# Performance work log

Measured on AMD Instinct MI355X. Metric: run time of the kernel, lower is better.

## Reference

```python
import jax, jax.numpy as jnp
import numpy as np

N_NODES = 100000
E_RAW = 3200000
IN_CH = 256
HID = 128
OUT = 64
N_LAYERS = 4


def setup_inputs() -> dict:
    rng = np.random.default_rng(0)
    src = rng.integers(0, N_NODES, E_RAW)
    dst = rng.integers(0, N_NODES, E_RAW)
    # drop self loops (add_self_loops appends them explicitly) and dedupe so the
    # edge list is coalesced (torch sparse .pow acts on coalesced values)
    code = src.astype(np.int64) * N_NODES + dst.astype(np.int64)
    code = np.unique(code[src != dst])
    edge_index = jnp.asarray(np.stack([code // N_NODES, code % N_NODES]), dtype=jnp.int32)

    key = jax.random.key(0)
    ks = jax.random.split(key, 6)
    stdv = 1.0 / np.sqrt(HID)
    x = jax.random.normal(ks[0], (N_NODES, IN_CH), jnp.float32)
    W_lin1 = jax.random.uniform(ks[1], (IN_CH, HID), jnp.float32, -stdv, stdv)
    b_lin1 = jnp.zeros((HID,), jnp.float32)
    W1 = jax.random.uniform(ks[2], (N_LAYERS, HID, HID), jnp.float32, -stdv, stdv)
    W2 = jax.random.uniform(ks[3], (N_LAYERS, HID, HID), jnp.float32, -stdv, stdv)
    W_lin2 = jax.random.uniform(ks[4], (HID, OUT), jnp.float32, -stdv, stdv)
    b_lin2 = jnp.zeros((OUT,), jnp.float32)
    return {"x": x, "W_lin1": W_lin1, "b_lin1": b_lin1, "W1": W1, "W2": W2,
            "W_lin2": W_lin2, "b_lin2": b_lin2, "edge_index": edge_index}


def reference(x, W_lin1, b_lin1, W1, W2, W_lin2, b_lin2, edge_index):
    n = N_NODES
    diag = jnp.arange(n, dtype=edge_index.dtype)
    # add self loops (appended last, so diagonal entries are the final n slots)
    row = jnp.concatenate([edge_index[0], diag])
    col = jnp.concatenate([edge_index[1], diag])
    deg = jax.ops.segment_sum(jnp.ones_like(row, jnp.float32), row, num_segments=n)
    inv_deg_row = 1.0 / deg[row]                     # per-edge 1/deg(src)
    a_vals = inv_deg_row                             # A_rw = D^{-1} A (incl. self loops)
    l_vals = (-inv_deg_row).at[-n:].add(1.0)         # L_rw = I - D^{-1} A (coalesced)

    def spmm(vals, X):
        return jax.ops.segment_sum(vals[:, None] * X[col], row, num_segments=n)

    h = jax.nn.relu(x @ W_lin1 + b_lin1)
    acc = jnp.zeros((n, HID), h.dtype)
    for l in range(N_LAYERS):
        o1 = h @ W1[l]
        o2 = h @ W2[l]
        if l != 0:
            # torch sparse .pow(l) = elementwise power of nonzero values
            o1 = spmm(l_vals ** l, o1)
            o2 = spmm(a_vals ** l, o2)
        if l != N_LAYERS - 1:
            o1 = spmm(a_vals, o1)
            o2 = spmm(l_vals, o2)
        acc = acc + jax.nn.relu(o1) + jax.nn.relu(o2)
    xm = acc / (2 * N_LAYERS)
    return xm @ W_lin2 + b_lin2
```

## Files before the change

### kernel.cpp

```cpp
#include <hip/hip_runtime.h>
#include <hip/hip_bf16.h>
#include <stdint.h>

#define NN   100000
#define ICH  256
#define HID  128
#define OUTF 64

typedef float  f32x4  __attribute__((ext_vector_type(4)));
typedef __bf16 bf16x8 __attribute__((ext_vector_type(8)));

__device__ __forceinline__ float bf2f(uint16_t u){
  union { uint32_t i; float f; } v; v.i = ((uint32_t)u) << 16; return v.f;
}
__device__ __forceinline__ uint16_t f2bf(float f){
  union { float f; uint32_t i; } v; v.f = f;
  uint32_t i = v.i;
  return (uint16_t)((i + 0x7FFFu + ((i >> 16) & 1u)) >> 16);
}
__device__ __forceinline__ uint32_t pack2(float a, float b){
  return (uint32_t)f2bf(a) | ((uint32_t)f2bf(b) << 16);
}

__global__ void k_csr(const int* __restrict__ row, int E, int n,
                      int* __restrict__ rp, float* __restrict__ r){
  int i = blockIdx.x * blockDim.x + threadIdx.x;
  if (i > n) return;
  int lo = 0, hi = E;
  while (lo < hi){
    int mid = (lo + hi) >> 1;
    if (row[mid] < i) lo = mid + 1; else hi = mid;
  }
  rp[i] = lo;
  if (i < n){
    int lo2 = lo, hi2 = E;
    while (lo2 < hi2){
      int mid = (lo2 + hi2) >> 1;
      if (row[mid] < i + 1) lo2 = mid + 1; else hi2 = mid;
    }
    r[i] = 1.0f / (float)(lo2 - lo + 1);
  }
}

__global__ void k_wprep(const float* __restrict__ W1, const float* __restrict__ W2,
                        const float* __restrict__ Wl1, const float* __restrict__ Wl2,
                        uint16_t* __restrict__ W1T, uint16_t* __restrict__ W2T,
                        uint16_t* __restrict__ Wl1T, uint16_t* __restrict__ Wl2T){
  int idx = blockIdx.x * blockDim.x + threadIdx.x;
  if (idx < 4 * 128 * 128){
    int l = idx >> 14, rem = idx & 16383, n = rem >> 7, k = rem & 127;
    W1T[idx] = f2bf(W1[l * 16384 + k * 128 + n]);
    W2T[idx] = f2bf(W2[l * 16384 + k * 128 + n]);
  }
  if (idx < 128 * 256){
    int n = idx >> 8, k = idx & 255;
    Wl1T[idx] = f2bf(Wl1[k * 128 + n]);
  }
  if (idx < 64 * 128){
    int n = idx >> 7, k = idx & 127;
    Wl2T[idx] = f2bf(Wl2[k * 64 + n]);
  }
}

__launch_bounds__(256)
__global__ void k_lin1m(const float* __restrict__ x, const uint16_t* __restrict__ Wl1T,
                        const float* __restrict__ b, uint16_t* __restrict__ h){
  __shared__ __align__(16) uint16_t Xs[64][264];
  const int tid = threadIdx.x;
  const int node0 = blockIdx.x * 64;
  const int wv = tid >> 6, lane = tid & 63, lr = lane & 15, lg = lane >> 4;

  #pragma unroll
  for (int i = 0; i < 16; ++i){
    int fi = tid + i * 256;
    int rrow = fi >> 6, c4 = (fi & 63) * 4;
    int nd = node0 + rrow;
    float4 f = (nd < NN) ? *(const float4*)(x + (size_t)nd * ICH + c4)
                         : make_float4(0.f, 0.f, 0.f, 0.f);
    *(uint2*)&Xs[rrow][c4] = make_uint2(pack2(f.x, f.y), pack2(f.z, f.w));
  }
  __syncthreads();

  bf16x8 bfr[2][8];
  #pragma unroll
  for (int n2 = 0; n2 < 2; ++n2){
    const int n = (2 * wv + n2) * 16 + lr;
    const uint16_t* bp = Wl1T + (size_t)n * 256 + lg * 8;
    #pragma unroll
    for (int ks = 0; ks < 8; ++ks)
      bfr[n2][ks] = __builtin_bit_cast(bf16x8, *(const uint4*)(bp + ks * 32));
  }
  float bias[2] = {b[(2 * wv + 0) * 16 + lr], b[(2 * wv + 1) * 16 + lr]};

  #pragma unroll
  for (int rt = 0; rt < 4; ++rt){
    const int row = rt * 16 + lr;
    bf16x8 af[8];
    #pragma unroll
    for (int ks = 0; ks < 8; ++ks)
      af[ks] = __builtin_bit_cast(bf16x8, *(const uint4*)&Xs[row][ks * 32 + lg * 8]);
    #pragma unroll
    for (int n2 = 0; n2 < 2; ++n2){
      f32x4 d = (f32x4){0.f, 0.f, 0.f, 0.f};
      #pragma unroll
      for (int ks = 0; ks < 8; ++ks)
        d = __builtin_amdgcn_mfma_f32_16x16x32_bf16(af[ks], bfr[n2][ks], d, 0, 0, 0);
      const int ncol = (2 * wv + n2) * 16 + lr;
      #pragma unroll
      for (int q = 0; q < 4; ++q){
        int nd = node0 + rt * 16 + lg * 4 + q;
        if (nd < NN){
          float v = d[q] + bias[n2];
          h[(size_t)nd * HID + ncol] = f2bf(v > 0.f ? v : 0.f);
        }
      }
    }
  }
}

__launch_bounds__(256)
__global__ void k_spmmA(const int* __restrict__ col, const int* __restrict__ rp,
                        const float* __restrict__ r, const uint32_t* __restrict__ h,
                        uint32_t* __restrict__ P, uint32_t* __restrict__ T1,
                        uint32_t* __restrict__ T2){
  int wid  = (blockIdx.x * blockDim.x + threadIdx.x) >> 6;
  int lane = threadIdx.x & 63;
  if (wid >= NN) return;
  int e0 = rp[wid], e1 = rp[wid + 1];
  float a0 = 0, b0 = 0, a1 = 0, b1 = 0, a2 = 0, b2 = 0;
  for (int base = e0; base < e1; base += 64){
    int tot = e1 - base;
    int cnt = tot < 64 ? tot : 64;
    int jv  = (lane < cnt) ? col[base + lane] : 0;
    int rvb = (lane < cnt) ? __builtin_bit_cast(int, r[jv]) : 0;
    int k = 0;
    if (cnt >= 16){
      uint32_t A[16], B[16];
      #pragma unroll
      for (int t = 0; t < 16; ++t){
        int j = __builtin_amdgcn_readlane(jv, t);
        A[t] = h[((uint32_t)j << 6) + lane];
      }
      while (k + 32 <= cnt){
        #pragma unroll
        for (int t = 0; t < 16; ++t){
          int j = __builtin_amdgcn_readlane(jv, k + 16 + t);
          B[t] = h[((uint32_t)j << 6) + lane];
        }
        #pragma unroll
        for (int t = 0; t < 16; ++t){
          float rj = __builtin_bit_cast(float, __builtin_amdgcn_readlane(rvb, k + t));
          float r2 = rj * rj;
          float x0 = __builtin_bit_cast(float, A[t] << 16);
          float x1 = __builtin_bit_cast(float, A[t] & 0xFFFF0000u);
          a0 += x0;               b0 += x1;
          a1 = fmaf(rj, x0, a1);  b1 = fmaf(rj, x1, b1);
          a2 = fmaf(r2, x0, a2);  b2 = fmaf(r2, x1, b2);
        }
        #pragma unroll
        for (int t = 0; t < 16; ++t) A[t] = B[t];
        k += 16;
      }
      #pragma unroll
      for (int t = 0; t < 16; ++t){
        float rj = __builtin_bit_cast(float, __builtin_amdgcn_readlane(rvb, k + t));
        float r2 = rj * rj;
        float x0 = __builtin_bit_cast(float, A[t] << 16);
        float x1 = __builtin_bit_cast(float, A[t] & 0xFFFF0000u);
        a0 += x0;               b0 += x1;
        a1 = fmaf(rj, x0, a1);  b1 = fmaf(rj, x1, b1);
        a2 = fmaf(r2, x0, a2);  b2 = fmaf(r2, x1, b2);
      }
      k += 16;
    }
    for (; k + 4 <= cnt; k += 4){
      uint32_t hv[4];
      #pragma unroll
      for (int t = 0; t < 4; ++t){
        int j = __builtin_amdgcn_readlane(jv, k + t);
        hv[t] = h[((uint32_t)j << 6) + lane];
      }
      #pragma unroll
      for (int t = 0; t < 4; ++t){
        float rj = __builtin_bit_cast(float, __builtin_amdgcn_readlane(rvb, k + t));
        float r2 = rj * rj;
        float x0 = __builtin_bit_cast(float, hv[t] << 16);
        float x1 = __builtin_bit_cast(float, hv[t] & 0xFFFF0000u);
        a0 += x0;               b0 += x1;
        a1 = fmaf(rj, x0, a1);  b1 = fmaf(rj, x1, b1);
        a2 = fmaf(r2, x0, a2);  b2 = fmaf(r2, x1, b2);
      }
    }
    for (; k < cnt; ++k){
      int j = __builtin_amdgcn_readlane(jv, k);
      float rj = __builtin_bit_cast(float, __builtin_amdgcn_readlane(rvb, k));
      float r2 = rj * rj;
      uint32_t hv = h[((uint32_t)j << 6) + lane];
      float x0 = __builtin_bit_cast(float, hv << 16);
      float x1 = __builtin_bit_cast(float, hv & 0xFFFF0000u);
      a0 += x0;               b0 += x1;
      a1 = fmaf(rj, x0, a1);  b1 = fmaf(rj, x1, b1);
      a2 = fmaf(r2, x0, a2);  b2 = fmaf(r2, x1, b2);
    }
  }
  size_t o = (size_t)wid * 64 + lane;
  P[o]  = pack2(a0, b0);
  T1[o] = pack2(a1, b1);
  T2[o] = pack2(a2, b2);
}

__launch_bounds__(256)
__global__ void k_spmmB(const int* __restrict__ col, const int* __restrict__ rp,
                        const float* __restrict__ r, const uint32_t* __restrict__ Pm,
                        uint32_t* __restrict__ Q1, uint32_t* __restrict__ Q2){
  int wid  = (blockIdx.x * blockDim.x + threadIdx.x) >> 6;
  int lane = threadIdx.x & 63;
  if (wid >= NN) return;
  int e0 = rp[wid], e1 = rp[wid + 1];
  float a1 = 0, b1 = 0, a2 = 0, b2 = 0;
  for (int base = e0; base < e1; base += 64){
    int tot = e1 - base;
    int cnt = tot < 64 ? tot : 64;
    int jv  = (lane < cnt) ? col[base + lane] : 0;
    int rvb = (lane < cnt) ? __builtin_bit_cast(int, r[jv]) : 0;
    int k = 0;
    if (cnt >= 16){
      uint32_t A[16], B[16];
      #pragma unroll
      for (int t = 0; t < 16; ++t){
        int j = __builtin_amdgcn_readlane(jv, t);
        A[t] = Pm[((uint32_t)j << 6) + lane];
      }
      while (k + 32 <= cnt){
        #pragma unroll
        for (int t = 0; t < 16; ++t){
          int j = __builtin_amdgcn_readlane(jv, k + 16 + t);
          B[t] = Pm[((uint32_t)j << 6) + lane];
        }
        #pragma unroll
        for (int t = 0; t < 16; ++t){
          float rj = __builtin_bit_cast(float, __builtin_amdgcn_readlane(rvb, k + t));
          float r2 = rj * rj;
          float x0 = __builtin_bit_cast(float, A[t] << 16);
          float x1 = __builtin_bit_cast(float, A[t] & 0xFFFF0000u);
          a1 = fmaf(rj, x0, a1);  b1 = fmaf(rj, x1, b1);
          a2 = fmaf(r2, x0, a2);  b2 = fmaf(r2, x1, b2);
        }
        #pragma unroll
        for (int t = 0; t < 16; ++t) A[t] = B[t];
        k += 16;
      }
      #pragma unroll
      for (int t = 0; t < 16; ++t){
        float rj = __builtin_bit_cast(float, __builtin_amdgcn_readlane(rvb, k + t));
        float r2 = rj * rj;
        float x0 = __builtin_bit_cast(float, A[t] << 16);
        float x1 = __builtin_bit_cast(float, A[t] & 0xFFFF0000u);
        a1 = fmaf(rj, x0, a1);  b1 = fmaf(rj, x1, b1);
        a2 = fmaf(r2, x0, a2);  b2 = fmaf(r2, x1, b2);
      }
      k += 16;
    }
    for (; k + 4 <= cnt; k += 4){
      uint32_t pv[4];
      #pragma unroll
      for (int t = 0; t < 4; ++t){
        int j = __builtin_amdgcn_readlane(jv, k + t);
        pv[t] = Pm[((uint32_t)j << 6) + lane];
      }
      #pragma unroll
      for (int t = 0; t < 4; ++t){
        float rj = __builtin_bit_cast(float, __builtin_amdgcn_readlane(rvb, k + t));
        float r2 = rj * rj;
        float x0 = __builtin_bit_cast(float, pv[t] << 16);
        float x1 = __builtin_bit_cast(float, pv[t] & 0xFFFF0000u);
        a1 = fmaf(rj, x0, a1);  b1 = fmaf(rj, x1, b1);
        a2 = fmaf(r2, x0, a2);  b2 = fmaf(r2, x1, b2);
      }
    }
    for (; k < cnt; ++k){
      int j = __builtin_amdgcn_readlane(jv, k);
      float rj = __builtin_bit_cast(float, __builtin_amdgcn_readlane(rvb, k));
      float r2 = rj * rj;
      uint32_t pv = Pm[((uint32_t)j << 6) + lane];
      float x0 = __builtin_bit_cast(float, pv << 16);
      float x1 = __builtin_bit_cast(float, pv & 0xFFFF0000u);
      a1 = fmaf(rj, x0, a1);  b1 = fmaf(rj, x1, b1);
      a2 = fmaf(r2, x0, a2);  b2 = fmaf(r2, x1, b2);
    }
  }
  size_t o = (size_t)wid * 64 + lane;
  Q1[o] = pack2(a1, b1);
  Q2[o] = pack2(a2, b2);
}

__launch_bounds__(512)
__global__ void k_epi8(const uint32_t* __restrict__ h,  const uint32_t* __restrict__ P,
                       const uint32_t* __restrict__ T1, const uint32_t* __restrict__ T2,
                       const uint32_t* __restrict__ Q1, const uint32_t* __restrict__ Q2,
                       const float* __restrict__ r,
                       const uint16_t* __restrict__ W1T, const uint16_t* __restrict__ W2T,
                       const uint16_t* __restrict__ Wl2T, const float* __restrict__ b2,
                       float* __restrict__ out){
  __shared__ __align__(16) uint32_t Mu[2][2][64][68];
  const int tid = threadIdx.x;
  const int node0 = blockIdx.x * 64;
  const int wv = tid >> 6, lane = tid & 63, lr = lane & 15, lg = lane >> 4;

  const int nb = tid >> 3;
  const int qc = tid & 7;
  const int nd = node0 + nb;
  const int rn = nd < NN ? nd : NN - 1;
  const float rv = r[rn];
  const size_t ub = (size_t)rn * 64;
  const int cc2[2] = {qc, qc + 8};

  f32x4 acc[4];
  #pragma unroll
  for (int rt = 0; rt < 4; ++rt) acc[rt] = (f32x4){0.f, 0.f, 0.f, 0.f};

  auto mfma_phase = [&](int buf, const uint16_t* Wa, const uint16_t* Wb){
    __builtin_amdgcn_s_setprio(1);
    #pragma unroll
    for (int m = 0; m < 2; ++m){
      const uint16_t* bp = (m ? Wb : Wa) + (size_t)(wv * 16 + lr) * 128 + lg * 8;
      bf16x8 bfr[4];
      #pragma unroll
      for (int ks = 0; ks < 4; ++ks)
        bfr[ks] = __builtin_bit_cast(bf16x8, *(const uint4*)(bp + ks * 32));
      #pragma unroll
      for (int rt = 0; rt < 4; ++rt){
        const int row = rt * 16 + lr;
        f32x4 d = (f32x4){0.f, 0.f, 0.f, 0.f};
        #pragma unroll
        for (int ks = 0; ks < 4; ++ks){
          bf16x8 af = __builtin_bit_cast(bf16x8,
              *(const uint4*)&Mu[buf][m][row][ks * 16 + lg * 4]);
          d = __builtin_amdgcn_mfma_f32_16x16x32_bf16(af, bfr[ks], d, 0, 0, 0);
        }
        #pragma unroll
        for (int q = 0; q < 4; ++q)
          acc[rt][q] += (d[q] > 0.f ? d[q] : 0.f);
      }
    }
    __builtin_amdgcn_s_setprio(0);
  };

  uint4 vh[2], vP[2], vT1[2], vQ1[2];
  #pragma unroll
  for (int ci = 0; ci < 2; ++ci){
    vh[ci]  = *(const uint4*)(h  + ub + cc2[ci] * 4);
    vP[ci]  = *(const uint4*)(P  + ub + cc2[ci] * 4);
    vT1[ci] = *(const uint4*)(T1 + ub + cc2[ci] * 4);
    vQ1[ci] = *(const uint4*)(Q1 + ub + cc2[ci] * 4);
  }

  #pragma unroll
  for (int ci = 0; ci < 2; ++ci){
    const uint32_t* ah = (const uint32_t*)&vh[ci];
    const uint32_t* ap = (const uint32_t*)&vP[ci];
    uint32_t o1[4], o2[4];
    #pragma unroll
    for (int w = 0; w < 4; ++w){
      float m1s[2], m2s[2];
      #pragma unroll
      for (int s = 0; s < 2; ++s){
        float hh = bf2f((uint16_t)(s ? (ah[w] >> 16) : ah[w]));
        float pp = bf2f((uint16_t)(s ? (ap[w] >> 16) : ap[w]));
        float F = rv * (pp + hh);
        m1s[s] = F; m2s[s] = hh - F;
      }
      o1[w] = pack2(m1s[0], m1s[1]);
      o2[w] = pack2(m2s[0], m2s[1]);
    }
    *(uint4*)&Mu[0][0][nb][cc2[ci] * 4] = make_uint4(o1[0], o1[1], o1[2], o1[3]);
    *(uint4*)&Mu[0][1][nb][cc2[ci] * 4] = make_uint4(o2[0], o2[1], o2[2], o2[3]);
  }
  __syncthreads();

  mfma_phase(0, W1T, W2T);
  #pragma unroll
  for (int ci = 0; ci < 2; ++ci){
    const uint32_t* ah = (const uint32_t*)&vh[ci];
    const uint32_t* ap = (const uint32_t*)&vP[ci];
    const uint32_t* at = (const uint32_t*)&vT1[ci];
    const uint32_t* aq = (const uint32_t*)&vQ1[ci];
    uint32_t o1[4], o2[4];
    #pragma unroll
    for (int w = 0; w < 4; ++w){
      float m1s[2], m2s[2];
      #pragma unroll
      for (int s = 0; s < 2; ++s){
        float hh = bf2f((uint16_t)(s ? (ah[w] >> 16) : ah[w]));
        float pp = bf2f((uint16_t)(s ? (ap[w] >> 16) : ap[w]));
        float t1 = bf2f((uint16_t)(s ? (at[w] >> 16) : at[w]));
        float q1 = bf2f((uint16_t)(s ? (aq[w] >> 16) : aq[w]));
        float F = rv * (pp + hh);
        float G = hh - F;
        m1s[s] = rv * (pp - q1 - t1 + G);
        m2s[s] = F - rv * (q1 + t1 + F);
      }
      o1[w] = pack2(m1s[0], m1s[1]);
      o2[w] = pack2(m2s[0], m2s[1]);
    }
    *(uint4*)&Mu[1][0][nb][cc2[ci] * 4] = make_uint4(o1[0], o1[1], o1[2], o1[3]);
    *(uint4*)&Mu[1][1][nb][cc2[ci] * 4] = make_uint4(o2[0], o2[1], o2[2], o2[3]);
  }
  uint4 vT2[2], vQ2[2];
  #pragma unroll
  for (int ci = 0; ci < 2; ++ci){
    vT2[ci] = *(const uint4*)(T2 + ub + cc2[ci] * 4);
    vQ2[ci] = *(const uint4*)(Q2 + ub + cc2[ci] * 4);
  }
  __syncthreads();

  mfma_phase(1, W1T + 16384, W2T + 16384);
  #pragma unroll
  for (int ci = 0; ci < 2; ++ci){
    const uint32_t* ah = (const uint32_t*)&vh[ci];
    const uint32_t* ap = (const uint32_t*)&vP[ci];
    const uint32_t* at1 = (const uint32_t*)&vT1[ci];
    const uint32_t* at2 = (const uint32_t*)&vT2[ci];
    const uint32_t* aq2 = (const uint32_t*)&vQ2[ci];
    uint32_t o1[4], o2[4];
    #pragma unroll
    for (int w = 0; w < 4; ++w){
      float m1s[2], m2s[2];
      #pragma unroll
      for (int s = 0; s < 2; ++s){
        float hh = bf2f((uint16_t)(s ? (ah[w] >> 16) : ah[w]));
        float pp = bf2f((uint16_t)(s ? (ap[w] >> 16) : ap[w]));
        float t1 = bf2f((uint16_t)(s ? (at1[w] >> 16) : at1[w]));
        float t2 = bf2f((uint16_t)(s ? (at2[w] >> 16) : at2[w]));
        float q2 = bf2f((uint16_t)(s ? (aq2[w] >> 16) : aq2[w]));
        float omr = 1.f - rv;
        float G2 = rv * rv * pp + omr * omr * hh;
        m1s[s] = rv * (q2 + pp - 2.f * t1 + t2 + G2);
        float F2 = rv * rv * (pp + hh);
        m2s[s] = F2 - rv * (q2 + t2 + F2);
      }
      o1[w] = pack2(m1s[0], m1s[1]);
      o2[w] = pack2(m2s[0], m2s[1]);
    }
    *(uint4*)&Mu[0][0][nb][cc2[ci] * 4] = make_uint4(o1[0], o1[1], o1[2], o1[3]);
    *(uint4*)&Mu[0][1][nb][cc2[ci] * 4] = make_uint4(o2[0], o2[1], o2[2], o2[3]);
  }
  __syncthreads();

  mfma_phase(0, W1T + 2 * 16384, W2T + 2 * 16384);
  #pragma unroll
  for (int ci = 0; ci < 2; ++ci){
    const uint32_t* ah = (const uint32_t*)&vh[ci];
    const uint32_t* ap = (const uint32_t*)&vP[ci];
    uint32_t o1[4], o2[4];
    #pragma unroll
    for (int w = 0; w < 4; ++w){
      float m1s[2], m2s[2];
      #pragma unroll
      for (int s = 0; s < 2; ++s){
        float hh = bf2f((uint16_t)(s ? (ah[w] >> 16) : ah[w]));
        float pp = bf2f((uint16_t)(s ? (ap[w] >> 16) : ap[w]));
        float omr = 1.f - rv;
        float r3 = rv * rv * rv;
        m1s[s] = omr * omr * omr * hh - r3 * pp;
        m2s[s] = r3 * (pp + hh);
      }
      o1[w] = pack2(m1s[0], m1s[1]);
      o2[w] = pack2(m2s[0], m2s[1]);
    }
    *(uint4*)&Mu[1][0][nb][cc2[ci] * 4] = make_uint4(o1[0], o1[1], o1[2], o1[3]);
    *(uint4*)&Mu[1][1][nb][cc2[ci] * 4] = make_uint4(o2[0], o2[1], o2[2], o2[3]);
  }
  __syncthreads();

  mfma_phase(1, W1T + 3 * 16384, W2T + 3 * 16384);

  uint16_t* Mb = (uint16_t*)&Mu[0][0][0][0];
  #pragma unroll
  for (int rt = 0; rt < 4; ++rt)
    #pragma unroll
    for (int q = 0; q < 4; ++q){
      int row = rt * 16 + lg * 4 + q;
      int colb = wv * 16 + lr;
      Mb[row * 136 + colb] = f2bf(acc[rt][q] * 0.125f);
    }
  __syncthreads();

  const int rt2 = wv >> 1;
  const int arow = rt2 * 16 + lr;
  bf16x8 af2[4];
  #pragma unroll
  for (int ks = 0; ks < 4; ++ks)
    af2[ks] = __builtin_bit_cast(bf16x8, *(const uint4*)&Mu[0][0][arow][ks * 16 + lg * 4]);
  #pragma unroll
  for (int ntl = 0; ntl < 2; ++ntl){
    const int nt = (wv & 1) * 2 + ntl;
    f32x4 d = (f32x4){0.f, 0.f, 0.f, 0.f};
    #pragma unroll
    for (int ks = 0; ks < 4; ++ks){
      bf16x8 bfr = __builtin_bit_cast(bf16x8,
          *(const uint4*)(Wl2T + (size_t)(nt * 16 + lr) * 128 + ks * 32 + lg * 8));
      d = __builtin_amdgcn_mfma_f32_16x16x32_bf16(af2[ks], bfr, d, 0, 0, 0);
    }
    float bias = b2[nt * 16 + lr];
    #pragma unroll
    for (int q = 0; q < 4; ++q){
      int rr = node0 + rt2 * 16 + lg * 4 + q;
      if (rr < NN) out[(size_t)rr * OUTF + nt * 16 + lr] = d[q] + bias;
    }
  }
}

extern "C" void kernel_launch(void* const* d_in, const int* in_sizes, int n_in,
                              void* d_out, int out_size, void* d_ws, size_t ws_size,
                              hipStream_t stream){
  const float* x   = (const float*)d_in[0];
  const float* Wl1 = (const float*)d_in[1];
  const float* bl1 = (const float*)d_in[2];
  const float* W1  = (const float*)d_in[3];
  const float* W2  = (const float*)d_in[4];
  const float* Wl2 = (const float*)d_in[5];
  const float* bl2 = (const float*)d_in[6];
  const int*   ei  = (const int*)d_in[7];
  int E = in_sizes[7] / 2;
  const int* rowp = ei;
  const int* colp = ei + E;

  char* ws = (char*)d_ws;
  size_t off = 0;
  auto alloc = [&](size_t bytes) -> void* {
    void* p = ws + off;
    off += (bytes + 255) & ~(size_t)255;
    return p;
  };
  const size_t MATB = (size_t)NN * HID * 2;
  uint32_t* h  = (uint32_t*)alloc(MATB);
  uint32_t* P  = (uint32_t*)alloc(MATB);
  uint32_t* T1 = (uint32_t*)alloc(MATB);
  uint32_t* T2 = (uint32_t*)alloc(MATB);
  uint32_t* Q1 = (uint32_t*)alloc(MATB);
  uint32_t* Q2 = (uint32_t*)alloc(MATB);
  float* r  = (float*)alloc((size_t)NN * 4);
  int* rp   = (int*)alloc((size_t)(NN + 1) * 4);
  uint16_t* W1T  = (uint16_t*)alloc((size_t)4 * 128 * 128 * 2);
  uint16_t* W2T  = (uint16_t*)alloc((size_t)4 * 128 * 128 * 2);
  uint16_t* Wl1T = (uint16_t*)alloc((size_t)128 * 256 * 2);
  uint16_t* Wl2T = (uint16_t*)alloc((size_t)64 * 128 * 2);

  k_wprep<<<(4 * 128 * 128 + 255) / 256, 256, 0, stream>>>(W1, W2, Wl1, Wl2,
                                                           W1T, W2T, Wl1T, Wl2T);
  k_csr<<<(NN + 1 + 255) / 256, 256, 0, stream>>>(rowp, E, NN, rp, r);
  k_lin1m<<<(NN + 63) / 64, 256, 0, stream>>>(x, Wl1T, bl1, (uint16_t*)h);
  k_spmmA<<<(NN + 3) / 4, 256, 0, stream>>>(colp, rp, r, h, P, T1, T2);
  k_spmmB<<<(NN + 3) / 4, 256, 0, stream>>>(colp, rp, r, P, Q1, Q2);
  k_epi8<<<(NN + 63) / 64, 512, 0, stream>>>(h, P, T1, T2, Q1, Q2, r,
                                             W1T, W2T, Wl2T, bl2, (float*)d_out);
}
```

Before: 408.5 us.

## Process four edges per wavefront with 16-byte gathers in SpMM kernels

Result: no change. 411.1 us (+0.6%).

```diff
diff --git a/kernel.cpp b/kernel.cpp
--- a/kernel.cpp
+++ b/kernel.cpp
@@ -126,87 +126,78 @@
   int wid  = (blockIdx.x * blockDim.x + threadIdx.x) >> 6;
   int lane = threadIdx.x & 63;
   if (wid >= NN) return;
+  const int g  = lane >> 4;
+  const uint32_t co = (uint32_t)(lane & 15) << 2;
   int e0 = rp[wid], e1 = rp[wid + 1];
-  float a0 = 0, b0 = 0, a1 = 0, b1 = 0, a2 = 0, b2 = 0;
+
+  float s0[8], s1[8], s2[8];
+  #pragma unroll
+  for (int u = 0; u < 8; ++u){ s0[u] = 0.f; s1[u] = 0.f; s2[u] = 0.f; }
+
   for (int base = e0; base < e1; base += 64){
     int tot = e1 - base;
     int cnt = tot < 64 ? tot : 64;
     int jv  = (lane < cnt) ? col[base + lane] : 0;
     int rvb = (lane < cnt) ? __builtin_bit_cast(int, r[jv]) : 0;
-    int k = 0;
-    if (cnt >= 16){
-      uint32_t A[16], B[16];
-      #pragma unroll
-      for (int t = 0; t < 16; ++t){
-        int j = __builtin_amdgcn_readlane(jv, t);
-        A[t] = h[((uint32_t)j << 6) + lane];
-      }
-      while (k + 32 <= cnt){
-        #pragma unroll
-        for (int t = 0; t < 16; ++t){
-          int j = __builtin_amdgcn_readlane(jv, k + 16 + t);
-          B[t] = h[((uint32_t)j << 6) + lane];
-        }
-        #pragma unroll
-        for (int t = 0; t < 16; ++t){
-          float rj = __builtin_bit_cast(float, __builtin_amdgcn_readlane(rvb, k + t));
-          float r2 = rj * rj;
-          float x0 = __builtin_bit_cast(float, A[t] << 16);
-          float x1 = __builtin_bit_cast(float, A[t] & 0xFFFF0000u);
-          a0 += x0;               b0 += x1;
-          a1 = fmaf(rj, x0, a1);  b1 = fmaf(rj, x1, b1);
-          a2 = fmaf(r2, x0, a2);  b2 = fmaf(r2, x1, b2);
-        }
-        #pragma unroll
-        for (int t = 0; t < 16; ++t) A[t] = B[t];
-        k += 16;
-      }
-      #pragma unroll
-      for (int t = 0; t < 16; ++t){
-        float rj = __builtin_bit_cast(float, __builtin_amdgcn_readlane(rvb, k + t));
-        float r2 = rj * rj;
-        float x0 = __builtin_bit_cast(float, A[t] << 16);
-        float x1 = __builtin_bit_cast(float, A[t] & 0xFFFF0000u);
-        a0 += x0;               b0 += x1;
-        a1 = fmaf(rj, x0, a1);  b1 = fmaf(rj, x1, b1);
-        a2 = fmaf(r2, x0, a2);  b2 = fmaf(r2, x1, b2);
-      }
-      k += 16;
-    }
-    for (; k + 4 <= cnt; k += 4){
-      uint32_t hv[4];
-      #pragma unroll
-      for (int t = 0; t < 4; ++t){
-        int j = __builtin_amdgcn_readlane(jv, k + t);
-        hv[t] = h[((uint32_t)j << 6) + lane];
-      }
-      #pragma unroll
-      for (int t = 0; t < 4; ++t){
-        float rj = __builtin_bit_cast(float, __builtin_amdgcn_readlane(rvb, k + t));
-        float r2 = rj * rj;
-        float x0 = __builtin_bit_cast(float, hv[t] << 16);
-        float x1 = __builtin_bit_cast(float, hv[t] & 0xFFFF0000u);
-        a0 += x0;               b0 += x1;
-        a1 = fmaf(rj, x0, a1);  b1 = fmaf(rj, x1, b1);
-        a2 = fmaf(r2, x0, a2);  b2 = fmaf(r2, x1, b2);
-      }
-    }
-    for (; k < cnt; ++k){
-      int j = __builtin_amdgcn_readlane(jv, k);
-      float rj = __builtin_bit_cast(float, __builtin_amdgcn_readlane(rvb, k));
-      float r2 = rj * rj;
-      uint32_t hv = h[((uint32_t)j << 6) + lane];
-      float x0 = __builtin_bit_cast(float, hv << 16);
-      float x1 = __builtin_bit_cast(float, hv & 0xFFFF0000u);
-      a0 += x0;               b0 += x1;
-      a1 = fmaf(rj, x0, a1);  b1 = fmaf(rj, x1, b1);
-      a2 = fmaf(r2, x0, a2);  b2 = fmaf(r2, x1, b2);
-    }
-  }
-  size_t o = (size_t)wid * 64 + lane;
-  P[o]  = pack2(a0, b0);
-  T1[o] = pack2(a1, b1);
-  T2[o] = pack2(a2, b2);
+    int kmax = (cnt + 3) & ~3;
+
+    int k = g;
+    int   jr = __shfl(jv, k);
+    float rr = __builtin_bit_cast(float, __shfl(rvb, k));
+    float wA = (k < cnt) ? 1.f : 0.f;
+    uint32_t jA = (k < cnt) ? (uint32_t)jr : 0u;
+    float rA = rr * wA;
+    uint4 A = *(const uint4*)(h + (jA << 6) + co);
+
+    for (k = g + 4; k < kmax; k += 4){
+      int   jr2 = __shfl(jv, k);
+      float rr2 = __builtin_bit_cast(float, __shfl(rvb, k));
+      float wB = (k < cnt) ? 1.f : 0.f;
+      uint32_t jB = (k < cnt) ? (uint32_t)jr2 : 0u;
+      float rB = rr2 * wB;
+      uint4 B = *(const uint4*)(h + (jB << 6) + co);
+
+      float r2 = rA * rA;
+      const uint32_t* au = (const uint32_t*)&A;
+      #pragma unroll
+      for (int u = 0; u < 4; ++u){
+        float x0 = __builtin_bit_cast(float, au[u] << 16);
+        float x1 = __builtin_bit_cast(float, au[u] & 0xFFFF0000u);
+        s0[2*u]   = fmaf(wA, x0, s0[2*u]);   s0[2*u+1] = fmaf(wA, x1, s0[2*u+1]);
+        s1[2*u]   = fmaf(rA, x0, s1[2*u]);   s1[2*u+1] = fmaf(rA, x1, s1[2*u+1]);
+        s2[2*u]   = fmaf(r2, x0, s2[2*u]);   s2[2*u+1] = fmaf(r2, x1, s2[2*u+1]);
+      }
+      A = B; wA = wB; rA = rB;
+    }
+    {
+      float r2 = rA * rA;
+      const uint32_t* au = (const uint32_t*)&A;
+      #pragma unroll
+      for (int u = 0; u < 4; ++u){
+        float x0 = __builtin_bit_cast(float, au[u] << 16);
+        float x1 = __builtin_bit_cast(float, au[u] & 0xFFFF0000u);
+        s0[2*u]   = fmaf(wA, x0, s0[2*u]);   s0[2*u+1] = fmaf(wA, x1, s0[2*u+1]);
+        s1[2*u]   = fmaf(rA, x0, s1[2*u]);   s1[2*u+1] = fmaf(rA, x1, s1[2*u+1]);
+        s2[2*u]   = fmaf(r2, x0, s2[2*u]);   s2[2*u+1] = fmaf(r2, x1, s2[2*u+1]);
+      }
+    }
+  }
+
+  #pragma unroll
+  for (int u = 0; u < 8; ++u){
+    s0[u] += __shfl_xor(s0[u], 16); s0[u] += __shfl_xor(s0[u], 32);
+    s1[u] += __shfl_xor(s1[u], 16); s1[u] += __shfl_xor(s1[u], 32);
+    s2[u] += __shfl_xor(s2[u], 16); s2[u] += __shfl_xor(s2[u], 32);
+  }
+  if (g == 0){
+    size_t o = ((size_t)wid << 6) + co;
+    *(uint4*)(P  + o) = make_uint4(pack2(s0[0], s0[1]), pack2(s0[2], s0[3]),
+                                   pack2(s0[4], s0[5]), pack2(s0[6], s0[7]));
+    *(uint4*)(T1 + o) = make_uint4(pack2(s1[0], s1[1]), pack2(s1[2], s1[3]),
+                                   pack2(s1[4], s1[5]), pack2(s1[6], s1[7]));
+    *(uint4*)(T2 + o) = make_uint4(pack2(s2[0], s2[1]), pack2(s2[2], s2[3]),
+                                   pack2(s2[4], s2[5]), pack2(s2[6], s2[7]));
+  }
 }
 
 __launch_bounds__(256)
@@ -216,82 +207,73 @@
   int wid  = (blockIdx.x * blockDim.x + threadIdx.x) >> 6;
   int lane = threadIdx.x & 63;
   if (wid >= NN) return;
+  const int g  = lane >> 4;
+  const uint32_t co = (uint32_t)(lane & 15) << 2;
   int e0 = rp[wid], e1 = rp[wid + 1];
-  float a1 = 0, b1 = 0, a2 = 0, b2 = 0;
+
+  float s1[8], s2[8];
+  #pragma unroll
+  for (int u = 0; u < 8; ++u){ s1[u] = 0.f; s2[u] = 0.f; }
+
   for (int base = e0; base < e1; base += 64){
     int tot = e1 - base;
     int cnt = tot < 64 ? tot : 64;
     int jv  = (lane < cnt) ? col[base + lane] : 0;
     int rvb = (lane < cnt) ? __builtin_bit_cast(int, r[jv]) : 0;
-    int k = 0;
-    if (cnt >= 16){
-      uint32_t A[16], B[16];
-      #pragma unroll
-      for (int t = 0; t < 16; ++t){
-        int j = __builtin_amdgcn_readlane(jv, t);
-        A[t] = Pm[((uint32_t)j << 6) + lane];
-      }
-      while (k + 32 <= cnt){
-        #pragma unroll
-        for (int t = 0; t < 16; ++t){
-          int j = __builtin_amdgcn_readlane(jv, k + 16 + t);
-          B[t] = Pm[((uint32_t)j << 6) + lane];
-        }
-        #pragma unroll
-        for (int t = 0; t < 16; ++t){
-          float rj = __builtin_bit_cast(float, __builtin_amdgcn_readlane(rvb, k + t));
-          float r2 = rj * rj;
-          float x0 = __builtin_bit_cast(float, A[t] << 16);
-          float x1 = __builtin_bit_cast(float, A[t] & 0xFFFF0000u);
-          a1 = fmaf(rj, x0, a1);  b1 = fmaf(rj, x1, b1);
-          a2 = fmaf(r2, x0, a2);  b2 = fmaf(r2, x1, b2);
-        }
-        #pragma unroll
-        for (int t = 0; t < 16; ++t) A[t] = B[t];
-        k += 16;
-      }
-      #pragma unroll
-      for (int t = 0; t < 16; ++t){
-        float rj = __builtin_bit_cast(float, __builtin_amdgcn_readlane(rvb, k + t));
-        float r2 = rj * rj;
-        float x0 = __builtin_bit_cast(float, A[t] << 16);
-        float x1 = __builtin_bit_cast(float, A[t] & 0xFFFF0000u);
-        a1 = fmaf(rj, x0, a1);  b1 = fmaf(rj, x1, b1);
-        a2 = fmaf(r2, x0, a2);  b2 = fmaf(r2, x1, b2);
-      }
-      k += 16;
-    }
-    for (; k + 4 <= cnt; k += 4){
-      uint32_t pv[4];
-      #pragma unroll
-      for (int t = 0; t < 4; ++t){
-        int j = __builtin_amdgcn_readlane(jv, k + t);
-        pv[t] = Pm[((uint32_t)j << 6) + lane];
-      }
-      #pragma unroll
-      for (int t = 0; t < 4; ++t){
-        float rj = __builtin_bit_cast(float, __builtin_amdgcn_readlane(rvb, k + t));
-        float r2 = rj * rj;
-        float x0 = __builtin_bit_cast(float, pv[t] << 16);
-        float x1 = __builtin_bit_cast(float, pv[t] & 0xFFFF0000u);
-        a1 = fmaf(rj, x0, a1);  b1 = fmaf(rj, x1, b1);
-        a2 = fmaf(r2, x0, a2);  b2 = fmaf(r2, x1, b2);
-      }
-    }
-    for (; k < cnt; ++k){
-      int j = __builtin_amdgcn_readlane(jv, k);
-      float rj = __builtin_bit_cast(float, __builtin_amdgcn_readlane(rvb, k));
-      float r2 = rj * rj;
-      uint32_t pv = Pm[((uint32_t)j << 6) + lane];
-      float x0 = __builtin_bit_cast(float, pv << 16);
-      float x1 = __builtin_bit_cast(float, pv & 0xFFFF0000u);
-      a1 = fmaf(rj, x0, a1);  b1 = fmaf(rj, x1, b1);
-      a2 = fmaf(r2, x0, a2);  b2 = fmaf(r2, x1, b2);
-    }
-  }
-  size_t o = (size_t)wid * 64 + lane;
-  Q1[o] = pack2(a1, b1);
-  Q2[o] = pack2(a2, b2);
+    int kmax = (cnt + 3) & ~3;
+
+    int k = g;
+    int   jr = __shfl(jv, k);
+    float rr = __builtin_bit_cast(float, __shfl(rvb, k));
+    float wA = (k < cnt) ? 1.f : 0.f;
+    uint32_t jA = (k < cnt) ? (uint32_t)jr : 0u;
+    float rA = rr * wA;
+    uint4 A = *(const uint4*)(Pm + (jA << 6) + co);
+
+    for (k = g + 4; k < kmax; k += 4){
+      int   jr2 = __shfl(jv, k);
+      float rr2 = __builtin_bit_cast(float, __shfl(rvb, k));
+      float wB = (k < cnt) ? 1.f : 0.f;
+      uint32_t jB = (k < cnt) ? (uint32_t)jr2 : 0u;
+      float rB = rr2 * wB;
+      uint4 B = *(const uint4*)(Pm + (jB << 6) + co);
+
+      float r2 = rA * rA;
+      const uint32_t* au = (const uint32_t*)&A;
+      #pragma unroll
+      for (int u = 0; u < 4; ++u){
+        float x0 = __builtin_bit_cast(float, au[u] << 16);
+        float x1 = __builtin_bit_cast(float, au[u] & 0xFFFF0000u);
+        s1[2*u] = fmaf(rA, x0, s1[2*u]);   s1[2*u+1] = fmaf(rA, x1, s1[2*u+1]);
+        s2[2*u] = fmaf(r2, x0, s2[2*u]);   s2[2*u+1] = fmaf(r2, x1, s2[2*u+1]);
+      }
+      A = B; rA = rB;
+    }
+    {
+      float r2 = rA * rA;
+      const uint32_t* au = (const uint32_t*)&A;
+      #pragma unroll
+      for (int u = 0; u < 4; ++u){
+        float x0 = __builtin_bit_cast(float, au[u] << 16);
+        float x1 = __builtin_bit_cast(float, au[u] & 0xFFFF0000u);
+        s1[2*u] = fmaf(rA, x0, s1[2*u]);   s1[2*u+1] = fmaf(rA, x1, s1[2*u+1]);
+        s2[2*u] = fmaf(r2, x0, s2[2*u]);   s2[2*u+1] = fmaf(r2, x1, s2[2*u+1]);
+      }
+    }
+  }
+
+  #pragma unroll
+  for (int u = 0; u < 8; ++u){
+    s1[u] += __shfl_xor(s1[u], 16); s1[u] += __shfl_xor(s1[u], 32);
+    s2[u] += __shfl_xor(s2[u], 16); s2[u] += __shfl_xor(s2[u], 32);
+  }
+  if (g == 0){
+    size_t o = ((size_t)wid << 6) + co;
+    *(uint4*)(Q1 + o) = make_uint4(pack2(s1[0], s1[1]), pack2(s1[2], s1[3]),
+                                   pack2(s1[4], s1[5]), pack2(s1[6], s1[7]));
+    *(uint4*)(Q2 + o) = make_uint4(pack2(s2[0], s2[1]), pack2(s2[2], s2[3]),
+                                   pack2(s2[4], s2[5]), pack2(s2[6], s2[7]));
+  }
 }
 
 __launch_bounds__(512)
```
